# Optimization experiments

Hardware: AMD Instinct MI355X
Metric: run time of the kernel (lower is better)

The kernel has to match this reference:

```python
import jax, jax.numpy as jnp
import numpy as np

NEG_SLOPE = 0.2  # PyG GATConv default negative_slope


def setup_inputs() -> dict:
    key = jax.random.key(0)
    k_x, k_e, k_w, k_as, k_ad = jax.random.split(key, 5)
    B, F, N, D, E, L = 2, 16, 5000, 128, 40000, 3
    x = jax.random.normal(k_x, (B, F, N, D), dtype=jnp.float32)
    edge_index = jax.random.randint(k_e, (B, F, 2, E), 0, N, dtype=jnp.int64)
    Ws = jax.random.normal(k_w, (L, D, D), dtype=jnp.float32) / np.float32(np.sqrt(D))
    att_src = jax.random.normal(k_as, (L, D), dtype=jnp.float32) / np.float32(np.sqrt(D))
    att_dst = jax.random.normal(k_ad, (L, D), dtype=jnp.float32) / np.float32(np.sqrt(D))
    bias = jnp.zeros((L, D), dtype=jnp.float32)
    return {"x": x, "edge_index": edge_index, "Ws": Ws,
            "att_src": att_src, "att_dst": att_dst, "bias": bias}


def _gat_layer(h, src, dst, n, W, a_s, a_d, b):
    # h: [n, D] node features; src/dst: [E_tot] edge endpoints (self-loops included)
    h2 = h @ W                                   # [n, D] transformed features
    s = h2 @ a_s                                 # [n] per-node source score
    d = h2 @ a_d                                 # [n] per-node dest score
    e = jax.nn.leaky_relu(s[src] + d[dst], NEG_SLOPE)   # [E_tot] raw attention
    m = jax.lax.stop_gradient(jax.ops.segment_max(e, dst, num_segments=n))
    ex = jnp.exp(e - m[dst])                     # numerically stable softmax per dst
    denom = jax.ops.segment_sum(ex, dst, num_segments=n)
    alpha = ex / denom[dst]                      # [E_tot] normalized attention
    out = jax.ops.segment_sum(alpha[:, None] * h2[src], dst, num_segments=n) + b
    return jax.nn.relu(out)


def reference(x, edge_index, Ws, att_src, att_dst, bias):
    B, F, N, D = x.shape
    n = B * F * N
    h = x.reshape(n, D)
    # faithful to torch: (BF,2,E).view(2,-1) is a raw row-major reshape
    ei = edge_index.reshape(2, -1)
    loop = jnp.arange(n, dtype=ei.dtype)         # PyG GATConv adds self-loops
    src = jnp.concatenate([ei[0], loop])
    dst = jnp.concatenate([ei[1], loop])
    for l in range(Ws.shape[0]):                 # fixed small layer loop
        h = _gat_layer(h, src, dst, n, Ws[l], att_src[l], att_dst[l], bias[l])
    return h.reshape(B, F, N, D)
```

## Files before the change

kernel.cpp:

```cpp
#include <hip/hip_runtime.h>
#include <math.h>

#define NODES_TOTAL 160000
#define NODES_REAL  5000
#define D 128
#define NEG 0.2f
#define KP2 128
#define HL2 (128 * KP2)
#define WT2_L (2 * HL2)

typedef unsigned short ushort_t;
typedef unsigned int uint_t;
typedef __attribute__((ext_vector_type(8))) __bf16 bf16x8;
typedef __attribute__((ext_vector_type(4))) float f32x4;
union BF8 { bf16x8 v; ushort_t u[8]; };

__device__ __forceinline__ void split2(float x, ushort_t& hi, ushort_t& lo) {
    unsigned u = __float_as_uint(x);
    hi = (ushort_t)(u >> 16);
    float hif = __uint_as_float(u & 0xffff0000u);
    lo = (ushort_t)(__float_as_uint(x - hif) >> 16);
}
__device__ __forceinline__ uint_t encmax(float f) {
    uint_t b = __float_as_uint(f);
    return b ^ ((uint_t)((int)b >> 31) | 0x80000000u);
}
__device__ __forceinline__ float decmax(uint_t u) {
    uint_t b = (u & 0x80000000u) ? (u ^ 0x80000000u) : ~u;
    return __uint_as_float(b);
}

__global__ void zero_kernel(int* counts, uint_t* gmaxu) {
    int i = blockIdx.x * blockDim.x + threadIdx.x;
    if (i < NODES_REAL) counts[i] = 0;
    if (i < 3) gmaxu[i] = 0u;
}

__global__ void rank_kernel(const int* __restrict__ ei, int* __restrict__ counts,
                            ushort_t* __restrict__ rank16, int Eh) {
    int e = blockIdx.x * blockDim.x + threadIdx.x;
    if (e < Eh) {
        int d = ei[Eh + e];
        int r = atomicAdd(&counts[d], 1);
        rank16[e] = (ushort_t)r;
    }
}

__global__ void scan_kernel(const int* __restrict__ counts, int* __restrict__ offs) {
    __shared__ int sd[1024];
    int t = threadIdx.x;
    int pre[5]; int sum = 0;
    #pragma unroll
    for (int u = 0; u < 5; ++u) {
        int idx = t * 5 + u;
        int c = (idx < NODES_REAL) ? counts[idx] : 0;
        pre[u] = sum; sum += c;
    }
    sd[t] = sum;
    __syncthreads();
    int run = sum;
    for (int o = 1; o < 1024; o <<= 1) {
        int v = (t >= o) ? sd[t - o] : 0;
        __syncthreads();
        sd[t] += v;
        __syncthreads();
    }
    int excl = sd[t] - run;
    #pragma unroll
    for (int u = 0; u < 5; ++u) {
        int idx = t * 5 + u;
        if (idx < NODES_REAL) offs[idx] = excl + pre[u];
    }
    if (t == 1023) offs[NODES_REAL] = excl + run;
}

__global__ void scatter_det(const int* __restrict__ ei, const int* __restrict__ offs,
                            const ushort_t* __restrict__ rank16, ushort_t* __restrict__ esrc,
                            int Eh) {
    int e = blockIdx.x * blockDim.x + threadIdx.x;
    if (e < Eh) {
        int s = ei[e];
        int d = ei[Eh + e];
        esrc[offs[d] + (int)rank16[e]] = (ushort_t)s;
    }
}

__global__ void wsplit_kernel(const float* __restrict__ Ws, ushort_t* __restrict__ Wt) {
    int l  = blockIdx.x >> 3;
    int n  = (blockIdx.x & 7) * 16 + (threadIdx.x >> 4);
    int c8 = threadIdx.x & 15;
    int k0 = c8 * 8;
    const float* src = Ws + (size_t)l * D * D;
    union { ushort_t u[8]; uint4 v; } hi, lo;
    #pragma unroll
    for (int j = 0; j < 8; ++j) split2(src[(size_t)(k0 + j) * D + n], hi.u[j], lo.u[j]);
    int c8s = c8 ^ (n & 15);
    ushort_t* dhi = Wt + (size_t)l * WT2_L + n * KP2 + c8s * 8;
    *(uint4*)dhi = hi.v;
    *(uint4*)(dhi + HL2) = lo.v;
}

__global__ __launch_bounds__(512)
void mlp3_kernel(const float* __restrict__ x, const ushort_t* __restrict__ Wt,
                 const float* __restrict__ bs, float* __restrict__ out) {
    __shared__ ushort_t Wl[WT2_L];
    __shared__ float scr[4][2][16][132];
    int tid = threadIdx.x;
    int w = tid >> 6, lane = tid & 63, q = lane >> 4, m16 = lane & 15;
    int p = w >> 1, h = w & 1;
    int row0 = NODES_REAL + blockIdx.x * 128 + p * 32;

    float4 xa[2][4][2];
    #pragma unroll
    for (int rt = 0; rt < 2; ++rt) {
        int r = row0 + rt * 16 + m16;
        if (r > NODES_TOTAL - 1) r = NODES_TOTAL - 1;
        #pragma unroll
        for (int kc = 0; kc < 4; ++kc) {
            const float* gp = x + (size_t)r * D + kc * 32 + q * 8;
            xa[rt][kc][0] = *(const float4*)gp;
            xa[rt][kc][1] = *(const float4*)(gp + 4);
        }
    }

    f32x4 acc[2][4];
    #pragma unroll
    for (int l = 0; l < 3; ++l) {
        __syncthreads();
        {
            const uint4* gw = (const uint4*)(Wt + (size_t)l * WT2_L);
            uint4* lw = (uint4*)Wl;
            #pragma unroll
            for (int r = 0; r < 8; ++r) lw[r * 512 + tid] = gw[r * 512 + tid];
        }
        if (l > 0) {
            #pragma unroll
            for (int rt = 0; rt < 2; ++rt)
                #pragma unroll
                for (int kc = 0; kc < 4; ++kc) {
                    const float* sp = &scr[p][rt][m16][kc * 32 + q * 8];
                    xa[rt][kc][0] = *(const float4*)sp;
                    xa[rt][kc][1] = *(const float4*)(sp + 4);
                }
        }
        __syncthreads();

        BF8 ahi[2][4], alo[2][4];
        #pragma unroll
        for (int rt = 0; rt < 2; ++rt)
            #pragma unroll
            for (int kc = 0; kc < 4; ++kc) {
                float4 v0 = xa[rt][kc][0], v1 = xa[rt][kc][1];
                float xv[8] = {v0.x, v0.y, v0.z, v0.w, v1.x, v1.y, v1.z, v1.w};
                #pragma unroll
                for (int j = 0; j < 8; ++j) split2(xv[j], ahi[rt][kc].u[j], alo[rt][kc].u[j]);
            }

        #pragma unroll
        for (int rt = 0; rt < 2; ++rt)
            #pragma unroll
            for (int ct = 0; ct < 4; ++ct) acc[rt][ct] = (f32x4){0.f, 0.f, 0.f, 0.f};

        const ushort_t* wbase = Wl + (h * 4) * (16 * KP2) + m16 * KP2;

        bf16x8 bh[2][4], bl[2][4];
        #pragma unroll
        for (int ct = 0; ct < 4; ++ct) {
            const ushort_t* bp = wbase + ct * (16 * KP2) + (((0 * 4 + q) ^ m16) * 8);
            bh[0][ct] = *(const bf16x8*)bp;
            bl[0][ct] = *(const bf16x8*)(bp + HL2);
        }
        #pragma unroll
        for (int kc = 0; kc < 4; ++kc) {
            int cur = kc & 1, nxt = cur ^ 1;
            if (kc < 3) {
                #pragma unroll
                for (int ct = 0; ct < 4; ++ct) {
                    const ushort_t* bp = wbase + ct * (16 * KP2) + ((((kc + 1) * 4 + q) ^ m16) * 8);
                    bh[nxt][ct] = *(const bf16x8*)bp;
                    bl[nxt][ct] = *(const bf16x8*)(bp + HL2);
                }
            }
            #pragma unroll
            for (int ct = 0; ct < 4; ++ct)
                #pragma unroll
                for (int rt = 0; rt < 2; ++rt) {
                    acc[rt][ct] = __builtin_amdgcn_mfma_f32_16x16x32_bf16(ahi[rt][kc].v, bh[cur][ct], acc[rt][ct], 0, 0, 0);
                    acc[rt][ct] = __builtin_amdgcn_mfma_f32_16x16x32_bf16(ahi[rt][kc].v, bl[cur][ct], acc[rt][ct], 0, 0, 0);
                    acc[rt][ct] = __builtin_amdgcn_mfma_f32_16x16x32_bf16(alo[rt][kc].v, bh[cur][ct], acc[rt][ct], 0, 0, 0);
                }
        }
        float bv[4];
        #pragma unroll
        for (int ct = 0; ct < 4; ++ct) bv[ct] = bs[l * D + (h * 4 + ct) * 16 + m16];
        #pragma unroll
        for (int rt = 0; rt < 2; ++rt)
            #pragma unroll
            for (int ct = 0; ct < 4; ++ct)
                #pragma unroll
                for (int reg = 0; reg < 4; ++reg)
                    scr[p][rt][q * 4 + reg][(h * 4 + ct) * 16 + m16] =
                        fmaxf(acc[rt][ct][reg] + bv[ct], 0.f);
    }
    __syncthreads();
    #pragma unroll
    for (int i = 0; i < 8; ++i) {
        int rowl = i * 2 + (lane >> 5);
        int grow = row0 + h * 16 + rowl;
        float4 v = *(const float4*)&scr[p][h][rowl][(lane & 31) * 4];
        if (grow < NODES_TOTAL)
            *(float4*)&out[(size_t)grow * D + (lane & 31) * 4] = v;
    }
}

__global__ __launch_bounds__(256)
void gsmall_kernel(const float* __restrict__ hin, const ushort_t* __restrict__ Wlg,
                   const float* __restrict__ a_s, const float* __restrict__ a_d,
                   float* __restrict__ h2, float* __restrict__ sv, float* __restrict__ dv,
                   uint_t* __restrict__ gmaxu) {
    __shared__ ushort_t Wl[WT2_L];
    int tid = threadIdx.x;
    {
        const uint4* gw = (const uint4*)Wlg;
        uint4* lw = (uint4*)Wl;
        #pragma unroll
        for (int r = 0; r < 16; ++r) lw[r * 256 + tid] = gw[r * 256 + tid];
    }
    int w = tid >> 6, lane = tid & 63, q = lane >> 4, m16 = lane & 15;
    int row0 = blockIdx.x * 128 + w * 32;
    f32x4 acc[2][8];
    #pragma unroll
    for (int rt = 0; rt < 2; ++rt)
        #pragma unroll
        for (int ct = 0; ct < 8; ++ct) acc[rt][ct] = (f32x4){0.f, 0.f, 0.f, 0.f};
    float4 xa[2][4][2];
    #pragma unroll
    for (int rt = 0; rt < 2; ++rt) {
        int r = row0 + rt * 16 + m16;
        if (r > NODES_REAL - 1) r = NODES_REAL - 1;
        #pragma unroll
        for (int kc = 0; kc < 4; ++kc) {
            const float* gp = hin + (size_t)r * D + kc * 32 + q * 8;
            xa[rt][kc][0] = *(const float4*)gp;
            xa[rt][kc][1] = *(const float4*)(gp + 4);
        }
    }
    __syncthreads();
    #pragma unroll
    for (int kc = 0; kc < 4; ++kc) {
        BF8 ahi[2], alo[2];
        #pragma unroll
        for (int rt = 0; rt < 2; ++rt) {
            float4 v0 = xa[rt][kc][0], v1 = xa[rt][kc][1];
            float xv[8] = {v0.x, v0.y, v0.z, v0.w, v1.x, v1.y, v1.z, v1.w};
            #pragma unroll
            for (int j = 0; j < 8; ++j) split2(xv[j], ahi[rt].u[j], alo[rt].u[j]);
        }
        #pragma unroll
        for (int ct = 0; ct < 8; ++ct) {
            const ushort_t* bp = Wl + (ct * 16 + m16) * KP2 + (((kc * 4 + q) ^ m16) * 8);
            bf16x8 bhi = *(const bf16x8*)bp;
            bf16x8 blo = *(const bf16x8*)(bp + HL2);
            #pragma unroll
            for (int rt = 0; rt < 2; ++rt) {
                acc[rt][ct] = __builtin_amdgcn_mfma_f32_16x16x32_bf16(ahi[rt].v, bhi, acc[rt][ct], 0, 0, 0);
                acc[rt][ct] = __builtin_amdgcn_mfma_f32_16x16x32_bf16(ahi[rt].v, blo, acc[rt][ct], 0, 0, 0);
                acc[rt][ct] = __builtin_amdgcn_mfma_f32_16x16x32_bf16(alo[rt].v, bhi, acc[rt][ct], 0, 0, 0);
            }
        }
    }
    #pragma unroll
    for (int rt = 0; rt < 2; ++rt)
        #pragma unroll
        for (int reg = 0; reg < 4; ++reg) {
            int grow = row0 + rt * 16 + q * 4 + reg;
            if (grow < NODES_REAL) {
                #pragma unroll
                for (int ct = 0; ct < 8; ++ct)
                    h2[(size_t)grow * D + ct * 16 + m16] = acc[rt][ct][reg];
            }
        }
    float asv[8], adv[8];
    #pragma unroll
    for (int ct = 0; ct < 8; ++ct) { asv[ct] = a_s[ct * 16 + m16]; adv[ct] = a_d[ct * 16 + m16]; }
    #pragma unroll
    for (int rt = 0; rt < 2; ++rt)
        #pragma unroll
        for (int reg = 0; reg < 4; ++reg) {
            float ps = 0.f, pd = 0.f;
            #pragma unroll
            for (int ct = 0; ct < 8; ++ct) {
                float v = acc[rt][ct][reg];
                ps += v * asv[ct]; pd += v * adv[ct];
            }
            #pragma unroll
            for (int o = 1; o < 16; o <<= 1) { ps += __shfl_xor(ps, o); pd += __shfl_xor(pd, o); }
            int grow = row0 + rt * 16 + q * 4 + reg;
            if (m16 == 0 && grow < NODES_REAL) {
                sv[grow] = ps; dv[grow] = pd;
                atomicMax(gmaxu, encmax(ps));
            }
        }
}

__global__ __launch_bounds__(256)
void agg_kernel(const float* __restrict__ h2, const float* __restrict__ sv,
                const float* __restrict__ dv, const int* __restrict__ offs,
                const ushort_t* __restrict__ esrc, const float* __restrict__ bias,
                float* __restrict__ out, const uint_t* __restrict__ gmaxu) {
    int w = threadIdx.x >> 6, lane = threadIdx.x & 63;
    int i = blockIdx.x * 4 + w;
    int start = offs[i], end = offs[i + 1];
    float d_i = dv[i];
    float gm = decmax(*gmaxu) + d_i;
    float m = gm > 0.f ? gm : NEG * gm;
    float ax = 0.f, ay = 0.f, ax1 = 0.f, ay1 = 0.f, exs = 0.f;
    for (int base = start; base < end; base += 64) {
        int cnt = min(64, end - base);
        int srci = (lane < cnt) ? (int)esrc[base + lane] : 0;
        float sc = sv[srci] + d_i;
        sc = sc > 0.f ? sc : NEG * sc;
        float ex = (lane < cnt) ? __expf(sc - m) : 0.f;
        exs += ex;
        if (cnt == 64) {
            #pragma unroll 4
            for (int j = 0; j < 64; j += 2) {
                int   s0 = __shfl(srci, j),     s1 = __shfl(srci, j + 1);
                float e0 = __shfl(ex, j),       e1 = __shfl(ex, j + 1);
                float2 h0 = *(const float2*)&h2[(size_t)s0 * D + 2 * lane];
                float2 h1 = *(const float2*)&h2[(size_t)s1 * D + 2 * lane];
                ax  += e0 * h0.x; ay  += e0 * h0.y;
                ax1 += e1 * h1.x; ay1 += e1 * h1.y;
            }
        } else {
            for (int j = 0; j < cnt; ++j) {
                int   src = __shfl(srci, j);
                float e   = __shfl(ex, j);
                float2 hv = *(const float2*)&h2[(size_t)src * D + 2 * lane];
                ax += e * hv.x; ay += e * hv.y;
            }
        }
    }
    ax += ax1; ay += ay1;
    float scf = sv[i] + d_i; scf = scf > 0.f ? scf : NEG * scf;
    float exf = __expf(scf - m);
    float2 hv = *(const float2*)&h2[(size_t)i * D + 2 * lane];
    ax += exf * hv.x; ay += exf * hv.y;
    #pragma unroll
    for (int o = 1; o < 64; o <<= 1) exs += __shfl_xor(exs, o);
    float rd = 1.f / (exs + exf);
    float2 b2 = *(const float2*)&bias[2 * lane];
    float2 o2 = make_float2(fmaxf(ax * rd + b2.x, 0.f), fmaxf(ay * rd + b2.y, 0.f));
    *(float2*)&out[(size_t)i * D + 2 * lane] = o2;
}

extern "C" void kernel_launch(void* const* d_in, const int* in_sizes, int n_in,
                              void* d_out, int out_size, void* d_ws, size_t ws_size,
                              hipStream_t stream) {
    const float* x   = (const float*)d_in[0];
    const int*   ei  = (const int*)d_in[1];
    const float* Ws  = (const float*)d_in[2];
    const float* as_ = (const float*)d_in[3];
    const float* ad_ = (const float*)d_in[4];
    const float* bs  = (const float*)d_in[5];
    float* out = (float*)d_out;
    int Eh = in_sizes[1] / 2;

    char* ws = (char*)d_ws;
    float*    h2     = (float*)ws;
    float*    bufS   = (float*)(ws + 2560000);
    float*    sv     = (float*)(ws + 5120000);
    float*    dv     = (float*)(ws + 5140000);
    int*      counts = (int*)  (ws + 5160000);
    int*      offs   = (int*)  (ws + 5180000);
    ushort_t* rank16 = (ushort_t*)(ws + 5200016);
    ushort_t* esrc   = (ushort_t*)(ws + 7760016);
    ushort_t* Wt     = (ushort_t*)(ws + 10320016);
    uint_t*   gmaxu  = (uint_t*)(ws + 10528912);

    zero_kernel<<<(NODES_REAL + 255) / 256, 256, 0, stream>>>(counts, gmaxu);
    rank_kernel<<<(Eh + 255) / 256, 256, 0, stream>>>(ei, counts, rank16, Eh);
    scan_kernel<<<1, 1024, 0, stream>>>(counts, offs);
    scatter_det<<<(Eh + 255) / 256, 256, 0, stream>>>(ei, offs, rank16, esrc, Eh);
    wsplit_kernel<<<24, 256, 0, stream>>>(Ws, Wt);

    mlp3_kernel<<<(NODES_TOTAL - NODES_REAL + 127) / 128, 512, 0, stream>>>(x, Wt, bs, out);

    for (int l = 0; l < 3; ++l) {
        const float* hin = (l == 0) ? x : bufS;
        float* hout = (l == 2) ? out : bufS;
        gsmall_kernel<<<(NODES_REAL + 127) / 128, 256, 0, stream>>>(
            hin, Wt + (size_t)l * WT2_L, as_ + l * D, ad_ + l * D, h2, sv, dv, gmaxu + l);
        agg_kernel<<<(NODES_REAL + 3) / 4, 256, 0, stream>>>(
            h2, sv, dv, offs, esrc, bs + l * D, hout, gmaxu + l);
    }
}
```

Baseline: 515.0 us.

## Read MFMA-fragment-ordered weights directly from global instead of staging in LDS

The weight split kernel now also writes the weights in a per-lane MFMA fragment order (Wm), and the MLP kernel loads B fragments straight from global/L2 instead of first copying the whole 64KB hi/lo weight matrix into shared memory each layer. The block shrinks to 256 threads covering 64 rows with launch_bounds(256,2), which cuts LDS use to the small activation scratch and should allow more resident blocks. The intent is to remove the per-layer LDS fill and its barriers. In exchange, every wave refetches weights from cache, roughly doubling weight traffic per row, and relies on L2 hit rates.

```diff
diff --git a/kernel.cpp b/kernel.cpp
--- a/kernel.cpp
+++ b/kernel.cpp
@@ -85,7 +85,8 @@
     }
 }
 
-__global__ void wsplit_kernel(const float* __restrict__ Ws, ushort_t* __restrict__ Wt) {
+__global__ void wsplit_kernel(const float* __restrict__ Ws, ushort_t* __restrict__ Wt,
+                              ushort_t* __restrict__ Wm) {
     int l  = blockIdx.x >> 3;
     int n  = (blockIdx.x & 7) * 16 + (threadIdx.x >> 4);
     int c8 = threadIdx.x & 15;
@@ -98,17 +99,21 @@
     ushort_t* dhi = Wt + (size_t)l * WT2_L + n * KP2 + c8s * 8;
     *(uint4*)dhi = hi.v;
     *(uint4*)(dhi + HL2) = lo.v;
-}
-
-__global__ __launch_bounds__(512)
-void mlp3_kernel(const float* __restrict__ x, const ushort_t* __restrict__ Wt,
+    int ct = n >> 4, m16 = n & 15, kc = c8 >> 2, qq = c8 & 3;
+    int lane = qq * 16 + m16;
+    ushort_t* d2 = Wm + (size_t)l * WT2_L + ((ct * 4 + kc) * 2 + 0) * 512 + lane * 8;
+    *(uint4*)d2 = hi.v;
+    *(uint4*)(d2 + 512) = lo.v;
+}
+
+__global__ __launch_bounds__(256, 2)
+void mlp3_kernel(const float* __restrict__ x, const ushort_t* __restrict__ Wm,
                  const float* __restrict__ bs, float* __restrict__ out) {
-    __shared__ ushort_t Wl[WT2_L];
-    __shared__ float scr[4][2][16][132];
+    __shared__ float scr[2][2][16][132];
     int tid = threadIdx.x;
     int w = tid >> 6, lane = tid & 63, q = lane >> 4, m16 = lane & 15;
     int p = w >> 1, h = w & 1;
-    int row0 = NODES_REAL + blockIdx.x * 128 + p * 32;
+    int row0 = NODES_REAL + blockIdx.x * 64 + p * 32;
 
     float4 xa[2][4][2];
     #pragma unroll
@@ -126,69 +131,53 @@
     f32x4 acc[2][4];
     #pragma unroll
     for (int l = 0; l < 3; ++l) {
-        __syncthreads();
-        {
-            const uint4* gw = (const uint4*)(Wt + (size_t)l * WT2_L);
-            uint4* lw = (uint4*)Wl;
-            #pragma unroll
-            for (int r = 0; r < 8; ++r) lw[r * 512 + tid] = gw[r * 512 + tid];
-        }
-        if (l > 0) {
-            #pragma unroll
-            for (int rt = 0; rt < 2; ++rt)
-                #pragma unroll
-                for (int kc = 0; kc < 4; ++kc) {
+        const ushort_t* Wml = Wm + (size_t)l * WT2_L;
+        if (l > 0) __syncthreads();
+
+        BF8 ahi[2][4], alo[2][4];
+        #pragma unroll
+        for (int rt = 0; rt < 2; ++rt)
+            #pragma unroll
+            for (int kc = 0; kc < 4; ++kc) {
+                float4 v0, v1;
+                if (l == 0) { v0 = xa[rt][kc][0]; v1 = xa[rt][kc][1]; }
+                else {
                     const float* sp = &scr[p][rt][m16][kc * 32 + q * 8];
-                    xa[rt][kc][0] = *(const float4*)sp;
-                    xa[rt][kc][1] = *(const float4*)(sp + 4);
+                    v0 = *(const float4*)sp; v1 = *(const float4*)(sp + 4);
                 }
-        }
-        __syncthreads();
-
-        BF8 ahi[2][4], alo[2][4];
+                float xv[8] = {v0.x, v0.y, v0.z, v0.w, v1.x, v1.y, v1.z, v1.w};
+                #pragma unroll
+                for (int j = 0; j < 8; ++j) split2(xv[j], ahi[rt][kc].u[j], alo[rt][kc].u[j]);
+            }
+        if (l > 0) __syncthreads();
+
         #pragma unroll
         for (int rt = 0; rt < 2; ++rt)
             #pragma unroll
-            for (int kc = 0; kc < 4; ++kc) {
-                float4 v0 = xa[rt][kc][0], v1 = xa[rt][kc][1];
-                float xv[8] = {v0.x, v0.y, v0.z, v0.w, v1.x, v1.y, v1.z, v1.w};
-                #pragma unroll
-                for (int j = 0; j < 8; ++j) split2(xv[j], ahi[rt][kc].u[j], alo[rt][kc].u[j]);
-            }
-
-        #pragma unroll
-        for (int rt = 0; rt < 2; ++rt)
-            #pragma unroll
             for (int ct = 0; ct < 4; ++ct) acc[rt][ct] = (f32x4){0.f, 0.f, 0.f, 0.f};
 
-        const ushort_t* wbase = Wl + (h * 4) * (16 * KP2) + m16 * KP2;
-
-        bf16x8 bh[2][4], bl[2][4];
-        #pragma unroll
-        for (int ct = 0; ct < 4; ++ct) {
-            const ushort_t* bp = wbase + ct * (16 * KP2) + (((0 * 4 + q) ^ m16) * 8);
-            bh[0][ct] = *(const bf16x8*)bp;
-            bl[0][ct] = *(const bf16x8*)(bp + HL2);
-        }
-        #pragma unroll
-        for (int kc = 0; kc < 4; ++kc) {
-            int cur = kc & 1, nxt = cur ^ 1;
-            if (kc < 3) {
-                #pragma unroll
-                for (int ct = 0; ct < 4; ++ct) {
-                    const ushort_t* bp = wbase + ct * (16 * KP2) + ((((kc + 1) * 4 + q) ^ m16) * 8);
-                    bh[nxt][ct] = *(const bf16x8*)bp;
-                    bl[nxt][ct] = *(const bf16x8*)(bp + HL2);
+        #pragma unroll
+        for (int ph = 0; ph < 2; ++ph) {
+            int kc0 = ph * 2;
+            bf16x8 bh[4][2], bl[4][2];
+            #pragma unroll
+            for (int ct = 0; ct < 4; ++ct)
+                #pragma unroll
+                for (int dk = 0; dk < 2; ++dk) {
+                    const ushort_t* bp = Wml + (((h * 4 + ct) * 4 + (kc0 + dk)) * 2) * 512 + lane * 8;
+                    bh[ct][dk] = *(const bf16x8*)bp;
+                    bl[ct][dk] = *(const bf16x8*)(bp + 512);
                 }
-            }
-            #pragma unroll
-            for (int ct = 0; ct < 4; ++ct)
-                #pragma unroll
-                for (int rt = 0; rt < 2; ++rt) {
-                    acc[rt][ct] = __builtin_amdgcn_mfma_f32_16x16x32_bf16(ahi[rt][kc].v, bh[cur][ct], acc[rt][ct], 0, 0, 0);
-                    acc[rt][ct] = __builtin_amdgcn_mfma_f32_16x16x32_bf16(ahi[rt][kc].v, bl[cur][ct], acc[rt][ct], 0, 0, 0);
-                    acc[rt][ct] = __builtin_amdgcn_mfma_f32_16x16x32_bf16(alo[rt][kc].v, bh[cur][ct], acc[rt][ct], 0, 0, 0);
-                }
+            #pragma unroll
+            for (int dk = 0; dk < 2; ++dk)
+                #pragma unroll
+                for (int ct = 0; ct < 4; ++ct)
+                    #pragma unroll
+                    for (int rt = 0; rt < 2; ++rt) {
+                        acc[rt][ct] = __builtin_amdgcn_mfma_f32_16x16x32_bf16(ahi[rt][kc0 + dk].v, bh[ct][dk], acc[rt][ct], 0, 0, 0);
+                        acc[rt][ct] = __builtin_amdgcn_mfma_f32_16x16x32_bf16(ahi[rt][kc0 + dk].v, bl[ct][dk], acc[rt][ct], 0, 0, 0);
+                        acc[rt][ct] = __builtin_amdgcn_mfma_f32_16x16x32_bf16(alo[rt][kc0 + dk].v, bh[ct][dk], acc[rt][ct], 0, 0, 0);
+                    }
         }
         float bv[4];
         #pragma unroll
@@ -377,14 +366,15 @@
     ushort_t* esrc   = (ushort_t*)(ws + 7760016);
     ushort_t* Wt     = (ushort_t*)(ws + 10320016);
     uint_t*   gmaxu  = (uint_t*)(ws + 10528912);
+    ushort_t* Wm     = (ushort_t*)(ws + 10528928);
 
     zero_kernel<<<(NODES_REAL + 255) / 256, 256, 0, stream>>>(counts, gmaxu);
     rank_kernel<<<(Eh + 255) / 256, 256, 0, stream>>>(ei, counts, rank16, Eh);
     scan_kernel<<<1, 1024, 0, stream>>>(counts, offs);
     scatter_det<<<(Eh + 255) / 256, 256, 0, stream>>>(ei, offs, rank16, esrc, Eh);
-    wsplit_kernel<<<24, 256, 0, stream>>>(Ws, Wt);
-
-    mlp3_kernel<<<(NODES_TOTAL - NODES_REAL + 127) / 128, 512, 0, stream>>>(x, Wt, bs, out);
+    wsplit_kernel<<<24, 256, 0, stream>>>(Ws, Wt, Wm);
+
+    mlp3_kernel<<<(NODES_TOTAL - NODES_REAL + 63) / 64, 256, 0, stream>>>(x, Wm, bs, out);
 
     for (int l = 0; l < 3; ++l) {
         const float* hin = (l == 0) ? x : bufS;
```

Measured after the change: 513.0 us. Within noise of the previous version (-0.4%).
